# Kernel optimization log

Measured on AMD Instinct MI355X. Metric: run time of the kernel, lower is better.

The kernel has to match this reference:

```python
import jax, jax.numpy as jnp
import numpy as np

BATCH = 512
IN_FLAT = 1024
NEURONS = 4096
FOCUS = 64


def setup_inputs() -> dict:
    key = jax.random.key(0)
    k1, k2, k3, k4 = jax.random.split(key, 4)
    x = jax.random.normal(k1, (BATCH, IN_FLAT), dtype=jnp.float32)
    connections_index = jax.random.randint(k2, (NEURONS, FOCUS), 0, IN_FLAT, dtype=jnp.int64)
    weights = jax.random.normal(k3, (NEURONS, FOCUS), dtype=jnp.float32)
    bias = jax.random.normal(k4, (NEURONS,), dtype=jnp.float32)
    return {"x": x, "connections_index": connections_index, "weights": weights, "bias": bias}


def reference(x, connections_index, weights, bias):
    # x: [B, IN_FLAT]; gather fixed sparse indices per output neuron
    # x_sel: [B, NEURONS, FOCUS]
    x_sel = jnp.take(x, connections_index, axis=1)
    # elementwise multiply by learned weights and reduce over focus dim
    y = jnp.sum(x_sel * weights, axis=-1) + bias  # [B, NEURONS]
    return y.reshape(x.shape[0], NEURONS)
```

## Files before the change

### kernel.cpp

```cpp
#include <hip/hip_runtime.h>

#define IN_FLAT 1024
#define BATCH   512
#define NEURONS 4096
#define FOCUS   64

typedef __bf16 bf16x8 __attribute__((ext_vector_type(8)));
typedef float  f32x4  __attribute__((ext_vector_type(4)));

__device__ __forceinline__ unsigned short f32_to_bf16(float f) {
    unsigned int u = __float_as_uint(f);
    unsigned int r = (u + 0x7fffu + ((u >> 16) & 1u)) >> 16;
    return (unsigned short)r;
}
__device__ __forceinline__ unsigned int pack2(float a, float b) {
    return (unsigned int)f32_to_bf16(a) | ((unsigned int)f32_to_bf16(b) << 16);
}

__global__ __launch_bounds__(256) void build_wt_kernel(
        const int* __restrict__ idx, const float* __restrict__ w,
        unsigned short* __restrict__ Wt) {
    __shared__ float rb[8 * IN_FLAT];
    const int t  = threadIdx.x;
    const int g0 = blockIdx.x * 8;

    float4* rb4 = reinterpret_cast<float4*>(rb);
    #pragma unroll
    for (int u = 0; u < 8; ++u)
        rb4[u * 256 + t] = float4{0.f, 0.f, 0.f, 0.f};
    __syncthreads();

    const int base = g0 * FOCUS;
    #pragma unroll
    for (int p = t; p < 8 * FOCUS; p += 256) {
        const int   i  = idx[base + p] & (IN_FLAT - 1);
        const float ww = w[base + p];
        atomicAdd(&rb[(p >> 6) * IN_FLAT + i], ww);
    }
    __syncthreads();

    uint4* dst = reinterpret_cast<uint4*>(Wt + (size_t)g0 * IN_FLAT);
    #pragma unroll
    for (int c = 0; c < 4; ++c) {
        const float4 lo = rb4[c * 512 + t * 2];
        const float4 hi = rb4[c * 512 + t * 2 + 1];
        dst[c * 256 + t] = uint4{pack2(lo.x, lo.y), pack2(lo.z, lo.w),
                                 pack2(hi.x, hi.y), pack2(hi.z, hi.w)};
    }
}

__global__ __launch_bounds__(256) void convert_x_kernel(
        const float* __restrict__ x, unsigned short* __restrict__ A) {
    const int t = blockIdx.x * 256 + threadIdx.x;
    const float4 lo = reinterpret_cast<const float4*>(x)[t * 2];
    const float4 hi = reinterpret_cast<const float4*>(x)[t * 2 + 1];
    reinterpret_cast<uint4*>(A)[t] = uint4{pack2(lo.x, lo.y), pack2(lo.z, lo.w),
                                           pack2(hi.x, hi.y), pack2(hi.z, hi.w)};
}

__global__ __launch_bounds__(256) void gemm_kernel(
        const unsigned short* __restrict__ A,
        const unsigned short* __restrict__ W,
        const float* __restrict__ bias,
        float* __restrict__ y) {
    __shared__ uint4 smem4[2048];
    char* smem = reinterpret_cast<char*>(smem4);

    const int b   = blockIdx.x;
    const int xcd = b & 7, jj = b >> 3;
    const int m0  = (jj & 7) * 64;
    const int n0  = (xcd * 8 + (jj >> 3)) * 64;

    const int tid  = threadIdx.x;
    const int lane = tid & 63;
    const int wv   = tid >> 6;
    const int wr   = wv >> 1, wc = wv & 1;

    const int s0 = tid * 16, s1 = s0 + 4096;
    const int r0 = s0 >> 7,  r1 = s1 >> 7;
    const int c0 = (s0 & 127) >> 1, c1 = (s1 & 127) >> 1;
    const unsigned short* gA0 = A + (m0 + r0) * IN_FLAT + c0;
    const unsigned short* gA1 = A + (m0 + r1) * IN_FLAT + c1;
    const unsigned short* gB0 = W + (size_t)(n0 + r0) * IN_FLAT + c0;
    const unsigned short* gB1 = W + (size_t)(n0 + r1) * IN_FLAT + c1;
    const int dA0 = s0 ^ ((r0 & 7) << 4);
    const int dA1 = s1 ^ ((r1 & 7) << 4);
    const int dB0 = dA0 + 8192, dB1 = dA1 + 8192;

    f32x4 acc[2][2] = {};
    uint4 ra0, ra1, rb0, rb1;

    ra0 = *reinterpret_cast<const uint4*>(gA0);
    ra1 = *reinterpret_cast<const uint4*>(gA1);
    rb0 = *reinterpret_cast<const uint4*>(gB0);
    rb1 = *reinterpret_cast<const uint4*>(gB1);

    for (int t = 0; t < IN_FLAT / 64; ++t) {
        const int bb = (t & 1) << 14;
        *reinterpret_cast<uint4*>(smem + bb + dA0) = ra0;
        *reinterpret_cast<uint4*>(smem + bb + dA1) = ra1;
        *reinterpret_cast<uint4*>(smem + bb + dB0) = rb0;
        *reinterpret_cast<uint4*>(smem + bb + dB1) = rb1;
        __syncthreads();

        if (t < 15) {
            const int k = (t + 1) * 64;
            ra0 = *reinterpret_cast<const uint4*>(gA0 + k);
            ra1 = *reinterpret_cast<const uint4*>(gA1 + k);
            rb0 = *reinterpret_cast<const uint4*>(gB0 + k);
            rb1 = *reinterpret_cast<const uint4*>(gB1 + k);
        }

        #pragma unroll
        for (int ks = 0; ks < 2; ++ks) {
            const int kb = ks * 64 + ((lane >> 4) << 4);
            bf16x8 af[2], bfr[2];
            #pragma unroll
            for (int fm = 0; fm < 2; ++fm) {
                const int row = wr * 32 + fm * 16 + (lane & 15);
                const int L   = row * 128 + kb;
                af[fm] = *reinterpret_cast<const bf16x8*>(
                    smem + bb + (L ^ ((row & 7) << 4)));
            }
            #pragma unroll
            for (int fn = 0; fn < 2; ++fn) {
                const int row = wc * 32 + fn * 16 + (lane & 15);
                const int L   = row * 128 + kb;
                bfr[fn] = *reinterpret_cast<const bf16x8*>(
                    smem + bb + 8192 + (L ^ ((row & 7) << 4)));
            }
            #pragma unroll
            for (int fm = 0; fm < 2; ++fm)
                #pragma unroll
                for (int fn = 0; fn < 2; ++fn)
                    acc[fm][fn] = __builtin_amdgcn_mfma_f32_16x16x32_bf16(
                        af[fm], bfr[fn], acc[fm][fn], 0, 0, 0);
        }
        __syncthreads();
    }

    const int nbase = n0 + wc * 32 + (lane & 15);
    const int mbase = m0 + wr * 32 + ((lane >> 4) << 2);
    #pragma unroll
    for (int fn = 0; fn < 2; ++fn) {
        const float bv = bias[nbase + fn * 16];
        #pragma unroll
        for (int fm = 0; fm < 2; ++fm) {
            #pragma unroll
            for (int jr = 0; jr < 4; ++jr) {
                y[(size_t)(mbase + fm * 16 + jr) * NEURONS + nbase + fn * 16] =
                    acc[fm][fn][jr] + bv;
            }
        }
    }
}

extern "C" void kernel_launch(void* const* d_in, const int* in_sizes, int n_in,
                              void* d_out, int out_size, void* d_ws, size_t ws_size,
                              hipStream_t stream) {
    const float* x    = (const float*)d_in[0];
    const int*   idx  = (const int*)  d_in[1];
    const float* w    = (const float*)d_in[2];
    const float* bias = (const float*)d_in[3];
    float*       y    = (float*)d_out;

    unsigned short* Wt = (unsigned short*)d_ws;
    unsigned short* A  = (unsigned short*)((char*)d_ws + (size_t)NEURONS * IN_FLAT * 2);

    build_wt_kernel<<<NEURONS / 8, 256, 0, stream>>>(idx, w, Wt);
    convert_x_kernel<<<BATCH * IN_FLAT / (256 * 8), 256, 0, stream>>>(x, A);
    gemm_kernel<<<(BATCH / 64) * (NEURONS / 64), 256, 0, stream>>>(A, Wt, bias, y);
}
```

Baseline: 82.22 us.

## Fuse dense weight build and x conversion into single sparse GEMM kernel

Replaces the three-kernel pipeline (scatter sparse weights into a dense bf16 matrix, convert x to bf16, GEMM) with one kernel. Each block holds its 64 neurons' indices and weights in registers, scatters each K-tile's slice into fp32 LDS with atomics, and converts both tiles to bf16 in LDS before the MFMA loop. This drops two launches and the global round trip of the 8 MB dense weight matrix and the bf16 copy of x. In exchange every block rebuilds its weight tiles, the LDS tile is now single-buffered with three barriers per iteration, and the global prefetch overlap of the old double buffer is reduced.

```diff
diff --git a/kernel.cpp b/kernel.cpp
--- a/kernel.cpp
+++ b/kernel.cpp
@@ -4,6 +4,11 @@
 #define BATCH   512
 #define NEURONS 4096
 #define FOCUS   64
+
+#define BF32_PITCH 68
+#define A16_BASE   17408
+#define B16_BASE   (17408 + 8192)
+#define LDS_TOTAL  (17408 + 8192 + 8192)
 
 typedef __bf16 bf16x8 __attribute__((ext_vector_type(8)));
 typedef float  f32x4  __attribute__((ext_vector_type(4)));
@@ -17,54 +22,14 @@
     return (unsigned int)f32_to_bf16(a) | ((unsigned int)f32_to_bf16(b) << 16);
 }
 
-__global__ __launch_bounds__(256) void build_wt_kernel(
-        const int* __restrict__ idx, const float* __restrict__ w,
-        unsigned short* __restrict__ Wt) {
-    __shared__ float rb[8 * IN_FLAT];
-    const int t  = threadIdx.x;
-    const int g0 = blockIdx.x * 8;
-
-    float4* rb4 = reinterpret_cast<float4*>(rb);
-    #pragma unroll
-    for (int u = 0; u < 8; ++u)
-        rb4[u * 256 + t] = float4{0.f, 0.f, 0.f, 0.f};
-    __syncthreads();
-
-    const int base = g0 * FOCUS;
-    #pragma unroll
-    for (int p = t; p < 8 * FOCUS; p += 256) {
-        const int   i  = idx[base + p] & (IN_FLAT - 1);
-        const float ww = w[base + p];
-        atomicAdd(&rb[(p >> 6) * IN_FLAT + i], ww);
-    }
-    __syncthreads();
-
-    uint4* dst = reinterpret_cast<uint4*>(Wt + (size_t)g0 * IN_FLAT);
-    #pragma unroll
-    for (int c = 0; c < 4; ++c) {
-        const float4 lo = rb4[c * 512 + t * 2];
-        const float4 hi = rb4[c * 512 + t * 2 + 1];
-        dst[c * 256 + t] = uint4{pack2(lo.x, lo.y), pack2(lo.z, lo.w),
-                                 pack2(hi.x, hi.y), pack2(hi.z, hi.w)};
-    }
-}
-
-__global__ __launch_bounds__(256) void convert_x_kernel(
-        const float* __restrict__ x, unsigned short* __restrict__ A) {
-    const int t = blockIdx.x * 256 + threadIdx.x;
-    const float4 lo = reinterpret_cast<const float4*>(x)[t * 2];
-    const float4 hi = reinterpret_cast<const float4*>(x)[t * 2 + 1];
-    reinterpret_cast<uint4*>(A)[t] = uint4{pack2(lo.x, lo.y), pack2(lo.z, lo.w),
-                                           pack2(hi.x, hi.y), pack2(hi.z, hi.w)};
-}
-
-__global__ __launch_bounds__(256) void gemm_kernel(
-        const unsigned short* __restrict__ A,
-        const unsigned short* __restrict__ W,
+__global__ __launch_bounds__(256) void fused_sparse_gemm_kernel(
+        const float* __restrict__ x,
+        const int*   __restrict__ idx,
+        const float* __restrict__ w,
         const float* __restrict__ bias,
-        float* __restrict__ y) {
-    __shared__ uint4 smem4[2048];
-    char* smem = reinterpret_cast<char*>(smem4);
+        float*       __restrict__ y) {
+    __shared__ char smem[LDS_TOTAL];
+    float* Bf32 = reinterpret_cast<float*>(smem);
 
     const int b   = blockIdx.x;
     const int xcd = b & 7, jj = b >> 3;
@@ -76,41 +41,84 @@
     const int wv   = tid >> 6;
     const int wr   = wv >> 1, wc = wv & 1;
 
-    const int s0 = tid * 16, s1 = s0 + 4096;
-    const int r0 = s0 >> 7,  r1 = s1 >> 7;
-    const int c0 = (s0 & 127) >> 1, c1 = (s1 & 127) >> 1;
-    const unsigned short* gA0 = A + (m0 + r0) * IN_FLAT + c0;
-    const unsigned short* gA1 = A + (m0 + r1) * IN_FLAT + c1;
-    const unsigned short* gB0 = W + (size_t)(n0 + r0) * IN_FLAT + c0;
-    const unsigned short* gB1 = W + (size_t)(n0 + r1) * IN_FLAT + c1;
-    const int dA0 = s0 ^ ((r0 & 7) << 4);
-    const int dA1 = s1 ^ ((r1 & 7) << 4);
-    const int dB0 = dA0 + 8192, dB1 = dA1 + 8192;
+    int   li[16];
+    float lw[16];
+    {
+        const int*   ip = idx + (size_t)n0 * FOCUS + tid * 4;
+        const float* wp = w   + (size_t)n0 * FOCUS + tid * 4;
+        #pragma unroll
+        for (int u = 0; u < 4; ++u) {
+            const int4   iv = *reinterpret_cast<const int4*>(ip + u * 1024);
+            const float4 wf = *reinterpret_cast<const float4*>(wp + u * 1024);
+            li[u*4+0] = iv.x & (IN_FLAT-1);  lw[u*4+0] = wf.x;
+            li[u*4+1] = iv.y & (IN_FLAT-1);  lw[u*4+1] = wf.y;
+            li[u*4+2] = iv.z & (IN_FLAT-1);  lw[u*4+2] = wf.z;
+            li[u*4+3] = iv.w & (IN_FLAT-1);  lw[u*4+3] = wf.w;
+        }
+    }
+    const int nrow_base = tid >> 4;
+
+    const int ar = tid >> 2, aq = tid & 3;
+    const float* xrow = x + (size_t)(m0 + ar) * IN_FLAT + aq * 16;
+    const int   aL0   = ar * 128 + aq * 32;
+    const int   swz   = (ar & 7) << 4;
+    char* adst0 = smem + A16_BASE + ((aL0     ) ^ swz);
+    char* adst1 = smem + A16_BASE + ((aL0 + 16) ^ swz);
+    char* bdst0 = smem + B16_BASE + ((aL0     ) ^ swz);
+    char* bdst1 = smem + B16_BASE + ((aL0 + 16) ^ swz);
+    const float* bsrc = Bf32 + ar * BF32_PITCH + aq * 16;
 
     f32x4 acc[2][2] = {};
-    uint4 ra0, ra1, rb0, rb1;
 
-    ra0 = *reinterpret_cast<const uint4*>(gA0);
-    ra1 = *reinterpret_cast<const uint4*>(gA1);
-    rb0 = *reinterpret_cast<const uint4*>(gB0);
-    rb1 = *reinterpret_cast<const uint4*>(gB1);
+    f32x4 pa0 = *reinterpret_cast<const f32x4*>(xrow + 0);
+    f32x4 pa1 = *reinterpret_cast<const f32x4*>(xrow + 4);
+    f32x4 pa2 = *reinterpret_cast<const f32x4*>(xrow + 8);
+    f32x4 pa3 = *reinterpret_cast<const f32x4*>(xrow + 12);
 
-    for (int t = 0; t < IN_FLAT / 64; ++t) {
-        const int bb = (t & 1) << 14;
-        *reinterpret_cast<uint4*>(smem + bb + dA0) = ra0;
-        *reinterpret_cast<uint4*>(smem + bb + dA1) = ra1;
-        *reinterpret_cast<uint4*>(smem + bb + dB0) = rb0;
-        *reinterpret_cast<uint4*>(smem + bb + dB1) = rb1;
+    for (int kt = 0; kt < IN_FLAT / 64; ++kt) {
+        {
+            const uint4 zz{0u, 0u, 0u, 0u};
+            uint4* z = reinterpret_cast<uint4*>(smem);
+            #pragma unroll
+            for (int u = 0; u < 4; ++u) z[u * 256 + tid] = zz;
+            if (tid < 64) z[1024 + tid] = zz;
+        }
         __syncthreads();
-
-        if (t < 15) {
-            const int k = (t + 1) * 64;
-            ra0 = *reinterpret_cast<const uint4*>(gA0 + k);
-            ra1 = *reinterpret_cast<const uint4*>(gA1 + k);
-            rb0 = *reinterpret_cast<const uint4*>(gB0 + k);
-            rb1 = *reinterpret_cast<const uint4*>(gB1 + k);
+        #pragma unroll
+        for (int u = 0; u < 4; ++u) {
+            #pragma unroll
+            for (int j = 0; j < 4; ++j) {
+                const int v = li[u*4+j];
+                if ((v >> 6) == kt)
+                    atomicAdd(&Bf32[(u*16 + nrow_base) * BF32_PITCH + (v & 63)],
+                              lw[u*4+j]);
+            }
         }
-
+        __syncthreads();
+        {
+            const f32x4 b0 = *reinterpret_cast<const f32x4*>(bsrc + 0);
+            const f32x4 b1 = *reinterpret_cast<const f32x4*>(bsrc + 4);
+            const f32x4 b2 = *reinterpret_cast<const f32x4*>(bsrc + 8);
+            const f32x4 b3 = *reinterpret_cast<const f32x4*>(bsrc + 12);
+            *reinterpret_cast<uint4*>(bdst0) =
+                uint4{pack2(b0[0], b0[1]), pack2(b0[2], b0[3]),
+                      pack2(b1[0], b1[1]), pack2(b1[2], b1[3])};
+            *reinterpret_cast<uint4*>(bdst1) =
+                uint4{pack2(b2[0], b2[1]), pack2(b2[2], b2[3]),
+                      pack2(b3[0], b3[1]), pack2(b3[2], b3[3])};
+            *reinterpret_cast<uint4*>(adst0) =
+                uint4{pack2(pa0[0], pa0[1]), pack2(pa0[2], pa0[3]),
+                      pack2(pa1[0], pa1[1]), pack2(pa1[2], pa1[3])};
+            *reinterpret_cast<uint4*>(adst1) =
+                uint4{pack2(pa2[0], pa2[1]), pack2(pa2[2], pa2[3]),
+                      pack2(pa3[0], pa3[1]), pack2(pa3[2], pa3[3])};
+            const int koff = (kt < 15) ? (kt + 1) * 64 : 0;
+            pa0 = *reinterpret_cast<const f32x4*>(xrow + koff + 0);
+            pa1 = *reinterpret_cast<const f32x4*>(xrow + koff + 4);
+            pa2 = *reinterpret_cast<const f32x4*>(xrow + koff + 8);
+            pa3 = *reinterpret_cast<const f32x4*>(xrow + koff + 12);
+        }
+        __syncthreads();
         #pragma unroll
         for (int ks = 0; ks < 2; ++ks) {
             const int kb = ks * 64 + ((lane >> 4) << 4);
@@ -120,14 +128,14 @@
                 const int row = wr * 32 + fm * 16 + (lane & 15);
                 const int L   = row * 128 + kb;
                 af[fm] = *reinterpret_cast<const bf16x8*>(
-                    smem + bb + (L ^ ((row & 7) << 4)));
+                    smem + A16_BASE + (L ^ ((row & 7) << 4)));
             }
             #pragma unroll
             for (int fn = 0; fn < 2; ++fn) {
                 const int row = wc * 32 + fn * 16 + (lane & 15);
                 const int L   = row * 128 + kb;
                 bfr[fn] = *reinterpret_cast<const bf16x8*>(
-                    smem + bb + 8192 + (L ^ ((row & 7) << 4)));
+                    smem + B16_BASE + (L ^ ((row & 7) << 4)));
             }
             #pragma unroll
             for (int fm = 0; fm < 2; ++fm)
@@ -136,7 +144,6 @@
                     acc[fm][fn] = __builtin_amdgcn_mfma_f32_16x16x32_bf16(
                         af[fm], bfr[fn], acc[fm][fn], 0, 0, 0);
         }
-        __syncthreads();
     }
 
     const int nbase = n0 + wc * 32 + (lane & 15);
@@ -164,10 +171,6 @@
     const float* bias = (const float*)d_in[3];
     float*       y    = (float*)d_out;
 
-    unsigned short* Wt = (unsigned short*)d_ws;
-    unsigned short* A  = (unsigned short*)((char*)d_ws + (size_t)NEURONS * IN_FLAT * 2);
-
-    build_wt_kernel<<<NEURONS / 8, 256, 0, stream>>>(idx, w, Wt);
-    convert_x_kernel<<<BATCH * IN_FLAT / (256 * 8), 256, 0, stream>>>(x, A);
-    gemm_kernel<<<(BATCH / 64) * (NEURONS / 64), 256, 0, stream>>>(A, Wt, bias, y);
+    fused_sparse_gemm_kernel<<<(BATCH / 64) * (NEURONS / 64), 256, 0, stream>>>(
+        x, idx, w, bias, y);
 }
```

After: 86.58 us. +5.3%, slower.
